# Kernel optimization log

Measured on AMD Instinct MI355X. Metric: run time of the kernel, lower is better.

Reference implementation:

```python
import jax, jax.numpy as jnp
import numpy as np

D = 128   # input_dim / num vars
LEAKY_SLOPE = 0.01  # torch F.leaky_relu default


def setup_inputs() -> dict:
    key = jax.random.key(0)
    ks = jax.random.split(key, 7)
    h, o, b = 64, 2, 8192
    scale = 0.05  # keep activations in a sane range
    return {
        "x": jax.random.normal(ks[0], (b, D), jnp.float32),
        "w0": jax.random.normal(ks[1], (D, h, D), jnp.float32) * scale,
        "w1": jax.random.normal(ks[2], (D, h, h), jnp.float32) * scale,
        "w2": jax.random.normal(ks[3], (D, o, h), jnp.float32) * scale,
        "b0": jax.random.normal(ks[4], (D, h), jnp.float32) * scale,
        "b1": jax.random.normal(ks[5], (D, h), jnp.float32) * scale,
        "b2": jax.random.normal(ks[6], (D, o), jnp.float32) * scale,
    }


def reference(x, w0, w1, w2, b0, b1, b2):
    # adjacency: all-ones minus identity (variable t cannot see itself)
    adj = jnp.ones((D, D), x.dtype) - jnp.eye(D, dtype=x.dtype)  # [j? no: (i,j)] symmetric
    # layer 0: out[b,t,i] = sum_j w0[t,i,j] * adj[j,t] * x[b,j]
    # mask the per-variable weights once, then a single contraction (no (t,i,j,b) intermediate)
    w0m = w0 * adj.T[:, None, :]            # (t,i,j); adj symmetric so adj[j,t]==adj[t,j]
    h = jnp.einsum('tij,bj->bti', w0m, x) + b0
    h = jax.nn.leaky_relu(h, LEAKY_SLOPE)
    # layer 1: per-variable dense
    h = jnp.einsum('tij,btj->bti', w1, h) + b1
    h = jax.nn.leaky_relu(h, LEAKY_SLOPE)
    # layer 2 (output, no nonlinearity)
    out = jnp.einsum('tij,btj->bti', w2, h) + b2  # (b, D, output_dim)
    # torch version returns torch.unbind(out, 1); stacked array carries same values
    return out
```

## Files before the change

### kernel.cpp

```cpp
#include <hip/hip_runtime.h>


typedef __bf16 bf16_t;
typedef __bf16 bf16x8 __attribute__((ext_vector_type(8)));
typedef float  f32x4  __attribute__((ext_vector_type(4)));
typedef __fp16 f16x2  __attribute__((ext_vector_type(2)));

#define LEAKY 0.01f

#define XB_OFF   0u
#define W0B_OFF  (2048u*1024u)
#define W1B_OFF  (4096u*1024u)

__global__ __launch_bounds__(256)
void brickify(const float* __restrict__ x,  const float* __restrict__ w0,
              const float* __restrict__ w1, unsigned char* __restrict__ ws)
{
    const int wid  = blockIdx.x * 4 + (threadIdx.x >> 6);
    const int lane = threadIdx.x & 63;
    const int lr = lane & 15, lq = lane >> 4;

    float v[8];
    if (wid < 2048) {
        int bt = wid >> 5, rem = wid & 31, nt = rem >> 2, ks = rem & 3;
        const float* s = x + (size_t)(bt*128 + nt*16 + lr) * 128 + ks*32 + lq*8;
        const float4 a = *(const float4*)s, b = *(const float4*)(s + 4);
        v[0]=a.x; v[1]=a.y; v[2]=a.z; v[3]=a.w;
        v[4]=b.x; v[5]=b.y; v[6]=b.z; v[7]=b.w;
    } else if (wid < 4096) {
        int u = wid - 2048, t = u >> 4, rem = u & 15, it = rem >> 2, ks = rem & 3;
        int k0 = ks*32 + lq*8;
        const float* s = w0 + (size_t)(t*64 + it*16 + lr) * 128 + k0;
        const float4 a = *(const float4*)s, b = *(const float4*)(s + 4);
        v[0]=a.x; v[1]=a.y; v[2]=a.z; v[3]=a.w;
        v[4]=b.x; v[5]=b.y; v[6]=b.z; v[7]=b.w;
        #pragma unroll
        for (int j = 0; j < 8; ++j) if (k0 + j == t) v[j] = 0.f;
    } else {
        int u = wid - 4096, t = u >> 3, rem = u & 7, it = rem >> 1, ks = rem & 1;
        const float* s = w1 + (size_t)(t*64 + it*16 + lr) * 64 + ks*32 + lq*8;
        const float4 a = *(const float4*)s, b = *(const float4*)(s + 4);
        v[0]=a.x; v[1]=a.y; v[2]=a.z; v[3]=a.w;
        v[4]=b.x; v[5]=b.y; v[6]=b.z; v[7]=b.w;
    }
    union { bf16_t h[8]; uint4 q; } pk;
    #pragma unroll
    for (int j = 0; j < 8; ++j) pk.h[j] = (bf16_t)v[j];
    ((uint4*)ws)[(size_t)wid * 64 + lane] = pk.q;
}

__global__ __launch_bounds__(256, 3)
void fused_mlp(const unsigned char* __restrict__ ws,
               const float* __restrict__ w2,
               const float* __restrict__ b0, const float* __restrict__ b1,
               const float* __restrict__ b2, float* __restrict__ out)
{
    __shared__ __align__(16) unsigned char hsm[8192];

    const int tid  = threadIdx.x;
    const int w    = tid >> 6;
    const int lane = tid & 63;
    const int lr = lane & 15, lq = lane >> 4;
    const int g  = blockIdx.x;
    const int t  = blockIdx.y;

    const unsigned char* w0p = ws + W0B_OFF + (size_t)t*16384 + lane*16;
    const unsigned char* w1p = ws + W1B_OFF + (size_t)t*8192  + lane*16;
    bf16x8 w0f[4][4], w1f[4][2];
    #pragma unroll
    for (int it = 0; it < 4; ++it)
        #pragma unroll
        for (int ks = 0; ks < 4; ++ks)
            w0f[it][ks] = *(const bf16x8*)(w0p + (it*4+ks)*1024);
    #pragma unroll
    for (int it = 0; it < 4; ++it)
        #pragma unroll
        for (int ks = 0; ks < 2; ++ks)
            w1f[it][ks] = *(const bf16x8*)(w1p + (it*2+ks)*1024);

    f16x2 w2h[2][4][2];
    #pragma unroll
    for (int o = 0; o < 2; ++o)
        #pragma unroll
        for (int it = 0; it < 4; ++it) {
            f32x4 v = *(const f32x4*)(w2 + t*128 + o*64 + it*16 + lq*4);
            w2h[o][it][0] = __builtin_amdgcn_cvt_pkrtz(v[0], v[1]);
            w2h[o][it][1] = __builtin_amdgcn_cvt_pkrtz(v[2], v[3]);
        }

    const float* b0p = b0 + t*64 + lq*4;
    const float* b1p = b1 + t*64 + lq*4;
    const float2 b2v = *(const float2*)(b2 + t*2);

    const unsigned char* xq = ws + XB_OFF + (size_t)(g*32 + w)*4096 + lane*16;
    bf16x8 xf[4];
    #pragma unroll
    for (int ks = 0; ks < 4; ++ks)
        xf[ks] = *(const bf16x8*)(xq + ks*1024);

    unsigned char* hb = hsm + w*2048;
    const int wboff = ((lq >> 1) * 16 + lr) * 16 + (lq & 1) * 8;

    for (int s = 0; s < 8; ++s) {
        f32x4 acc[4];
        #pragma unroll
        for (int it = 0; it < 4; ++it)
            acc[it] = *(const f32x4*)(b0p + it*16);
        #pragma unroll
        for (int ks = 0; ks < 4; ++ks)
            #pragma unroll
            for (int it = 0; it < 4; ++it)
                acc[it] = __builtin_amdgcn_mfma_f32_16x16x32_bf16(
                              w0f[it][ks], xf[ks], acc[it], 0, 0, 0);

        {
            const unsigned char* xn = xq + (s < 7 ? (s + 1) : 7) * 16384;
            #pragma unroll
            for (int ks = 0; ks < 4; ++ks)
                xf[ks] = *(const bf16x8*)(xn + ks*1024);
        }

        #pragma unroll
        for (int it = 0; it < 4; ++it) {
            union { bf16_t h[4]; unsigned long long u; } pk;
            #pragma unroll
            for (int r = 0; r < 4; ++r) {
                float u = acc[it][r];
                pk.h[r] = (bf16_t)fmaxf(u, LEAKY * u);
            }
            *(unsigned long long*)(hb + (it>>1)*1024 + (it&1)*512 + wboff) = pk.u;
        }

        bf16x8 hf0 = *(const bf16x8*)(hb + lane*16);
        bf16x8 hf1 = *(const bf16x8*)(hb + 1024 + lane*16);
        #pragma unroll
        for (int it = 0; it < 4; ++it)
            acc[it] = *(const f32x4*)(b1p + it*16);
        #pragma unroll
        for (int it = 0; it < 4; ++it) {
            acc[it] = __builtin_amdgcn_mfma_f32_16x16x32_bf16(
                          w1f[it][0], hf0, acc[it], 0, 0, 0);
            acc[it] = __builtin_amdgcn_mfma_f32_16x16x32_bf16(
                          w1f[it][1], hf1, acc[it], 0, 0, 0);
        }

        float p0 = 0.f, p1 = 0.f;
        #pragma unroll
        for (int it = 0; it < 4; ++it) {
            #pragma unroll
            for (int p = 0; p < 2; ++p) {
                float u0 = acc[it][2*p],   v0 = fmaxf(u0, LEAKY * u0);
                float u1 = acc[it][2*p+1], v1 = fmaxf(u1, LEAKY * u1);
                f16x2 hh = __builtin_amdgcn_cvt_pkrtz(v0, v1);
                p0 = __builtin_amdgcn_fdot2(w2h[0][it][p], hh, p0, false);
                p1 = __builtin_amdgcn_fdot2(w2h[1][it][p], hh, p1, false);
            }
        }
        p0 += __shfl_xor(p0, 16); p0 += __shfl_xor(p0, 32);
        p1 += __shfl_xor(p1, 16); p1 += __shfl_xor(p1, 32);
        if (lq == 0) {
            int row = g*512 + s*64 + w*16 + lr;
            float2 o2 = { p0 + b2v.x, p1 + b2v.y };
            *(float2*)(out + (size_t)row*256 + t*2) = o2;
        }
    }
}

extern "C" void kernel_launch(void* const* d_in, const int* in_sizes, int n_in,
                              void* d_out, int out_size, void* d_ws, size_t ws_size,
                              hipStream_t stream) {
    const float* x  = (const float*)d_in[0];
    const float* w0 = (const float*)d_in[1];
    const float* w1 = (const float*)d_in[2];
    const float* w2 = (const float*)d_in[3];
    const float* b0 = (const float*)d_in[4];
    const float* b1 = (const float*)d_in[5];
    const float* b2 = (const float*)d_in[6];
    unsigned char* ws = (unsigned char*)d_ws;
    float* out = (float*)d_out;

    brickify<<<dim3(1280), dim3(256), 0, stream>>>(x, w0, w1, ws);
    fused_mlp<<<dim3(16, 128), dim3(256), 0, stream>>>(ws, w2, b0, b1, b2, out);
}
```

Before: 113.8 us.

## Split hidden units across wave pairs with async LDS x staging

```diff
diff --git a/kernel.cpp b/kernel.cpp
--- a/kernel.cpp
+++ b/kernel.cpp
@@ -11,6 +11,12 @@
 #define XB_OFF   0u
 #define W0B_OFF  (2048u*1024u)
 #define W1B_OFF  (4096u*1024u)
+
+__device__ __forceinline__ void async_copy16(void* lds, const void* g) {
+    __builtin_amdgcn_global_load_lds(
+        (const __attribute__((address_space(1))) unsigned int*)g,
+        (__attribute__((address_space(3))) unsigned int*)lds, 16, 0, 0);
+}
 
 __global__ __launch_bounds__(256)
 void brickify(const float* __restrict__ x,  const float* __restrict__ w0,
@@ -49,16 +55,20 @@
     ((uint4*)ws)[(size_t)wid * 64 + lane] = pk.q;
 }
 
-__global__ __launch_bounds__(256, 3)
+__global__ __launch_bounds__(256, 4)
 void fused_mlp(const unsigned char* __restrict__ ws,
                const float* __restrict__ w2,
                const float* __restrict__ b0, const float* __restrict__ b1,
                const float* __restrict__ b2, float* __restrict__ out)
 {
-    __shared__ __align__(16) unsigned char hsm[8192];
+    __shared__ __align__(1024) unsigned char xsm[16384];
+    __shared__ __align__(1024) unsigned char hsm[8192];
+    __shared__ __align__(16)   float psm[2][2][2][16][2];
 
     const int tid  = threadIdx.x;
-    const int w    = tid >> 6;
+    const int wv   = tid >> 6;
+    const int pair = wv >> 1;
+    const int half = wv & 1;
     const int lane = tid & 63;
     const int lr = lane & 15, lq = lane >> 4;
     const int g  = blockIdx.x;
@@ -66,103 +76,126 @@
 
     const unsigned char* w0p = ws + W0B_OFF + (size_t)t*16384 + lane*16;
     const unsigned char* w1p = ws + W1B_OFF + (size_t)t*8192  + lane*16;
-    bf16x8 w0f[4][4], w1f[4][2];
-    #pragma unroll
-    for (int it = 0; it < 4; ++it)
+    bf16x8 w0f[2][4], w1f[2][2];
+    #pragma unroll
+    for (int itl = 0; itl < 2; ++itl) {
+        const int it = half*2 + itl;
         #pragma unroll
         for (int ks = 0; ks < 4; ++ks)
-            w0f[it][ks] = *(const bf16x8*)(w0p + (it*4+ks)*1024);
-    #pragma unroll
-    for (int it = 0; it < 4; ++it)
+            w0f[itl][ks] = *(const bf16x8*)(w0p + (it*4+ks)*1024);
         #pragma unroll
         for (int ks = 0; ks < 2; ++ks)
-            w1f[it][ks] = *(const bf16x8*)(w1p + (it*2+ks)*1024);
-
-    f16x2 w2h[2][4][2];
+            w1f[itl][ks] = *(const bf16x8*)(w1p + (it*2+ks)*1024);
+    }
+    f16x2 w2h[2][2][2];
     #pragma unroll
     for (int o = 0; o < 2; ++o)
         #pragma unroll
-        for (int it = 0; it < 4; ++it) {
-            f32x4 v = *(const f32x4*)(w2 + t*128 + o*64 + it*16 + lq*4);
-            w2h[o][it][0] = __builtin_amdgcn_cvt_pkrtz(v[0], v[1]);
-            w2h[o][it][1] = __builtin_amdgcn_cvt_pkrtz(v[2], v[3]);
-        }
-
-    const float* b0p = b0 + t*64 + lq*4;
-    const float* b1p = b1 + t*64 + lq*4;
+        for (int itl = 0; itl < 2; ++itl) {
+            f32x4 v = *(const f32x4*)(w2 + t*128 + o*64 + (half*2+itl)*16 + lq*4);
+            w2h[o][itl][0] = __builtin_amdgcn_cvt_pkrtz(v[0], v[1]);
+            w2h[o][itl][1] = __builtin_amdgcn_cvt_pkrtz(v[2], v[3]);
+        }
+    f32x4 b0q[2], b1q[2];
+    #pragma unroll
+    for (int itl = 0; itl < 2; ++itl) {
+        b0q[itl] = *(const f32x4*)(b0 + t*64 + (half*2+itl)*16 + lq*4);
+        b1q[itl] = *(const f32x4*)(b1 + t*64 + (half*2+itl)*16 + lq*4);
+    }
     const float2 b2v = *(const float2*)(b2 + t*2);
 
-    const unsigned char* xq = ws + XB_OFF + (size_t)(g*32 + w)*4096 + lane*16;
-    bf16x8 xf[4];
-    #pragma unroll
-    for (int ks = 0; ks < 4; ++ks)
-        xf[ks] = *(const bf16x8*)(xq + ks*1024);
-
-    unsigned char* hb = hsm + w*2048;
+    const unsigned char* xsrc0 = ws + XB_OFF + (size_t)(g*16 + pair)*4096 + lane*16;
+    unsigned char* xd0 = xsm + pair*8192;
     const int wboff = ((lq >> 1) * 16 + lr) * 16 + (lq & 1) * 8;
 
+    if (half == 0) {
+        #pragma unroll
+        for (int c = 0; c < 4; ++c)
+            async_copy16(xd0 + c*1024, xsrc0 + c*1024);
+        #pragma unroll
+        for (int c = 0; c < 4; ++c)
+            async_copy16(xd0 + 4096 + c*1024, xsrc0 + 2*4096 + c*1024);
+    }
+    __syncthreads();
+
     for (int s = 0; s < 8; ++s) {
-        f32x4 acc[4];
-        #pragma unroll
-        for (int it = 0; it < 4; ++it)
-            acc[it] = *(const f32x4*)(b0p + it*16);
-        #pragma unroll
-        for (int ks = 0; ks < 4; ++ks)
-            #pragma unroll
-            for (int it = 0; it < 4; ++it)
-                acc[it] = __builtin_amdgcn_mfma_f32_16x16x32_bf16(
-                              w0f[it][ks], xf[ks], acc[it], 0, 0, 0);
-
-        {
-            const unsigned char* xn = xq + (s < 7 ? (s + 1) : 7) * 16384;
-            #pragma unroll
-            for (int ks = 0; ks < 4; ++ks)
-                xf[ks] = *(const bf16x8*)(xn + ks*1024);
-        }
-
-        #pragma unroll
-        for (int it = 0; it < 4; ++it) {
+        const unsigned char* xb = xsm + pair*8192 + (s&1)*4096 + lane*16;
+        f32x4 acc[2];
+        acc[0] = b0q[0]; acc[1] = b0q[1];
+        #pragma unroll
+        for (int ks = 0; ks < 4; ++ks) {
+            bf16x8 xk = *(const bf16x8*)(xb + ks*1024);
+            acc[0] = __builtin_amdgcn_mfma_f32_16x16x32_bf16(w0f[0][ks], xk, acc[0], 0, 0, 0);
+            acc[1] = __builtin_amdgcn_mfma_f32_16x16x32_bf16(w0f[1][ks], xk, acc[1], 0, 0, 0);
+        }
+
+        unsigned char* hb = hsm + pair*4096 + (s&1)*2048;
+        #pragma unroll
+        for (int itl = 0; itl < 2; ++itl) {
             union { bf16_t h[4]; unsigned long long u; } pk;
             #pragma unroll
             for (int r = 0; r < 4; ++r) {
-                float u = acc[it][r];
+                float u = acc[itl][r];
                 pk.h[r] = (bf16_t)fmaxf(u, LEAKY * u);
             }
-            *(unsigned long long*)(hb + (it>>1)*1024 + (it&1)*512 + wboff) = pk.u;
+            *(unsigned long long*)(hb + half*1024 + itl*512 + wboff) = pk.u;
+        }
+
+        __syncthreads();
+
+        if (s > 0 && half == 0 && lq == 0) {
+            const int pb = (s-1) & 1;
+            float2 pa = *(const float2*)&psm[pb][pair][0][lr][0];
+            float2 pc = *(const float2*)&psm[pb][pair][1][lr][0];
+            int row = (g*16 + (s-1)*2 + pair)*16 + lr;
+            float2 o2 = { pa.x + pc.x + b2v.x, pa.y + pc.y + b2v.y };
+            *(float2*)(out + (size_t)row*256 + t*2) = o2;
+        }
+
+        if (half == 0 && s + 2 < 8) {
+            const unsigned char* xs = xsrc0 + (size_t)(s+2)*2*4096;
+            unsigned char* xd = xd0 + (s&1)*4096;
+            #pragma unroll
+            for (int c = 0; c < 4; ++c)
+                async_copy16(xd + c*1024, xs + c*1024);
         }
 
         bf16x8 hf0 = *(const bf16x8*)(hb + lane*16);
         bf16x8 hf1 = *(const bf16x8*)(hb + 1024 + lane*16);
-        #pragma unroll
-        for (int it = 0; it < 4; ++it)
-            acc[it] = *(const f32x4*)(b1p + it*16);
-        #pragma unroll
-        for (int it = 0; it < 4; ++it) {
-            acc[it] = __builtin_amdgcn_mfma_f32_16x16x32_bf16(
-                          w1f[it][0], hf0, acc[it], 0, 0, 0);
-            acc[it] = __builtin_amdgcn_mfma_f32_16x16x32_bf16(
-                          w1f[it][1], hf1, acc[it], 0, 0, 0);
+        acc[0] = b1q[0]; acc[1] = b1q[1];
+        #pragma unroll
+        for (int itl = 0; itl < 2; ++itl) {
+            acc[itl] = __builtin_amdgcn_mfma_f32_16x16x32_bf16(w1f[itl][0], hf0, acc[itl], 0, 0, 0);
+            acc[itl] = __builtin_amdgcn_mfma_f32_16x16x32_bf16(w1f[itl][1], hf1, acc[itl], 0, 0, 0);
         }
 
         float p0 = 0.f, p1 = 0.f;
         #pragma unroll
-        for (int it = 0; it < 4; ++it) {
+        for (int itl = 0; itl < 2; ++itl) {
             #pragma unroll
             for (int p = 0; p < 2; ++p) {
-                float u0 = acc[it][2*p],   v0 = fmaxf(u0, LEAKY * u0);
-                float u1 = acc[it][2*p+1], v1 = fmaxf(u1, LEAKY * u1);
+                float u0 = acc[itl][2*p],   v0 = fmaxf(u0, LEAKY * u0);
+                float u1 = acc[itl][2*p+1], v1 = fmaxf(u1, LEAKY * u1);
                 f16x2 hh = __builtin_amdgcn_cvt_pkrtz(v0, v1);
-                p0 = __builtin_amdgcn_fdot2(w2h[0][it][p], hh, p0, false);
-                p1 = __builtin_amdgcn_fdot2(w2h[1][it][p], hh, p1, false);
+                p0 = __builtin_amdgcn_fdot2(w2h[0][itl][p], hh, p0, false);
+                p1 = __builtin_amdgcn_fdot2(w2h[1][itl][p], hh, p1, false);
             }
         }
         p0 += __shfl_xor(p0, 16); p0 += __shfl_xor(p0, 32);
         p1 += __shfl_xor(p1, 16); p1 += __shfl_xor(p1, 32);
         if (lq == 0) {
-            int row = g*512 + s*64 + w*16 + lr;
-            float2 o2 = { p0 + b2v.x, p1 + b2v.y };
-            *(float2*)(out + (size_t)row*256 + t*2) = o2;
-        }
+            float2 pv = { p0, p1 };
+            *(float2*)&psm[s&1][pair][half][lr][0] = pv;
+        }
+    }
+
+    __syncthreads();
+    if (half == 0 && lq == 0) {
+        float2 pa = *(const float2*)&psm[1][pair][0][lr][0];
+        float2 pc = *(const float2*)&psm[1][pair][1][lr][0];
+        int row = (g*16 + 7*2 + pair)*16 + lr;
+        float2 o2 = { pa.x + pc.x + b2v.x, pa.y + pc.y + b2v.y };
+        *(float2*)(out + (size_t)row*256 + t*2) = o2;
     }
 }
 
@@ -180,5 +213,5 @@
     float* out = (float*)d_out;
 
     brickify<<<dim3(1280), dim3(256), 0, stream>>>(x, w0, w1, ws);
-    fused_mlp<<<dim3(16, 128), dim3(256), 0, stream>>>(ws, w2, b0, b1, b2, out);
-}
+    fused_mlp<<<dim3(32, 128), dim3(256), 0, stream>>>(ws, w2, b0, b1, b2, out);
+}
```

Measured after the change: 113.8 us. Within noise of the previous version (+0.0%).
